# Kernel optimization log

Hardware: AMD Instinct MI355X
Metric: run time of the kernel (lower is better)

Reference implementation:

```python
import jax, jax.numpy as jnp
import numpy as np

N_NODES = 50000
N_EDGES = 800000
D = 128


def setup_inputs() -> dict:
    key = jax.random.key(0)
    ks = jax.random.split(key, 8)
    # xavier-uniform bound for [D, D]
    bound = np.sqrt(6.0 / (D + D)).astype(np.float32)
    x = jax.random.normal(ks[0], (N_NODES, D), dtype=jnp.float32)
    edge_index = jax.random.randint(ks[1], (2, N_EDGES), 0, N_NODES)
    W0 = jax.random.uniform(ks[2], (D, D), jnp.float32, -bound, bound)
    W1 = jax.random.uniform(ks[3], (D, D), jnp.float32, -bound, bound)
    W2 = jax.random.uniform(ks[4], (D, D), jnp.float32, -bound, bound)
    b0 = jnp.zeros((D,), jnp.float32)
    b1 = jnp.zeros((D,), jnp.float32)
    b2 = jnp.zeros((D,), jnp.float32)
    return {"x": x, "edge_index": edge_index,
            "W0": W0, "b0": b0, "W1": W1, "b1": b1, "W2": W2, "b2": b2}


def _gcn_conv(h, W, b, row, col, norm, n):
    # PyG GCNConv: x' = hat(D)^-1/2 hat(A) hat(D)^-1/2 (h W) + b
    hw = h @ W                                   # [N, D]
    msg = norm[:, None] * hw[row]                # gather from source nodes
    agg = jax.ops.segment_sum(msg, col, num_segments=n)  # scatter-add to targets
    return agg + b


def reference(x, edge_index, W0, b0, W1, b1, W2, b2):
    n = x.shape[0]
    loops = jnp.arange(n)
    # add self-loops (PyG GCNConv default)
    row = jnp.concatenate([edge_index[0], loops])
    col = jnp.concatenate([edge_index[1], loops])
    deg = jax.ops.segment_sum(jnp.ones(row.shape, x.dtype), col, num_segments=n)
    dinv = jnp.where(deg > 0, jax.lax.rsqrt(deg), 0.0)
    norm = dinv[row] * dinv[col]
    # dropout omitted (eval/inference mode)
    res = []
    h = x
    for W, b in ((W0, b0), (W1, b1), (W2, b2)):
        h = jnp.tanh(_gcn_conv(h, W, b, row, col, norm, n))
        res.append(h)
    return jnp.stack(res, axis=1)  # [N, n_layers, D]
```

## Files before the change

kernel.cpp:

```cpp
#include <hip/hip_runtime.h>
#include <math.h>

#define N_NODES 50000
#define N_EDGES 800000
#define D 128
#define NPAD 50048
#define NBLK 196

typedef unsigned int uint32;
typedef __attribute__((ext_vector_type(8))) short short8;
typedef __attribute__((ext_vector_type(4))) float f32x4;

__device__ __forceinline__ ushort f2bf(float f) {
    uint32 u = __float_as_uint(f);
    u = (u + 0x7fff + ((u >> 16) & 1)) >> 16;
    return (ushort)u;
}
__device__ __forceinline__ float bf2f(ushort u) {
    return __uint_as_float(((uint32)u) << 16);
}


__global__ __launch_bounds__(256) void k_count(const int* __restrict__ col,
                                               int* __restrict__ counts,
                                               int* __restrict__ rank_buf) {
    int i4 = (blockIdx.x * 256 + threadIdx.x) * 4;
    if (i4 < N_EDGES) {
        int4 c = *(const int4*)(col + i4);
        int4 r;
        r.x = atomicAdd(&counts[c.x], 1);
        r.y = atomicAdd(&counts[c.y], 1);
        r.z = atomicAdd(&counts[c.z], 1);
        r.w = atomicAdd(&counts[c.w], 1);
        *(int4*)(rank_buf + i4) = r;
    }
}

__global__ __launch_bounds__(256) void k_scan_local(const int* __restrict__ counts,
                                                    int* __restrict__ offsets,
                                                    int* __restrict__ partials) {
    __shared__ int wsum[4];
    int tid = threadIdx.x;
    int i = blockIdx.x * 256 + tid;
    int v = (i < N_NODES) ? counts[i] : 0;
    int lane = tid & 63, wv = tid >> 6;
    int x = v;
    #pragma unroll
    for (int off = 1; off < 64; off <<= 1) {
        int y = __shfl_up(x, off);
        if (lane >= off) x += y;
    }
    if (lane == 63) wsum[wv] = x;
    __syncthreads();
    int b0 = wsum[0], b1 = wsum[1], b2 = wsum[2], b3 = wsum[3];
    int base = (wv > 0 ? b0 : 0) + (wv > 1 ? b1 : 0) + (wv > 2 ? b2 : 0);
    if (i < N_NODES) offsets[i] = base + x - v;
    if (tid == 255) partials[blockIdx.x] = b0 + b1 + b2 + b3;
}

__global__ __launch_bounds__(256) void k_scan_add(int* __restrict__ offsets,
                                                  const int* __restrict__ partials,
                                                  const int* __restrict__ counts,
                                                  float* __restrict__ dinv) {
    __shared__ int wsum[4];
    int tid = threadIdx.x;
    int p = (tid < (int)blockIdx.x && tid < NBLK) ? partials[tid] : 0;
    int lane = tid & 63, wv = tid >> 6;
    #pragma unroll
    for (int off = 32; off; off >>= 1) p += __shfl_down(p, off);
    if (lane == 0) wsum[wv] = p;
    __syncthreads();
    int base = wsum[0] + wsum[1] + wsum[2] + wsum[3];
    int i = blockIdx.x * 256 + tid;
    if (i < N_NODES) {
        offsets[i] += base;
        dinv[i] = rsqrtf((float)counts[i] + 1.0f);
    }
    if (i == 0) offsets[N_NODES] = N_EDGES;
}

__global__ __launch_bounds__(256) void k_fill(const int* __restrict__ row,
                                              const int* __restrict__ col,
                                              const int* __restrict__ offsets,
                                              const int* __restrict__ rank_buf,
                                              int* __restrict__ csr_rows) {
    int i4 = (blockIdx.x * 256 + threadIdx.x) * 4;
    if (i4 < N_EDGES) {
        int4 c = *(const int4*)(col + i4);
        int4 r = *(const int4*)(rank_buf + i4);
        int4 rw = *(const int4*)(row + i4);
        csr_rows[offsets[c.x] + r.x] = rw.x;
        csr_rows[offsets[c.y] + r.y] = rw.y;
        csr_rows[offsets[c.z] + r.z] = rw.z;
        csr_rows[offsets[c.w] + r.w] = rw.w;
    }
}

#define BM 64
#define LDA 136
#define NTILES ((N_NODES + BM - 1) / BM)
#define GEMM_BLOCKS 512

__global__ __launch_bounds__(256) void k_gemm(const float* __restrict__ hf,
                                              const ushort* __restrict__ hb,
                                              const float* __restrict__ W,
                                              const float* __restrict__ dinv,
                                              ushort* __restrict__ hw) {
    __shared__ __align__(16) ushort As[BM * LDA];
    __shared__ __align__(16) ushort Wt[D * LDA];
    int tid = threadIdx.x;
    int lane = tid & 63;
    int w = tid >> 6;
    int quad = lane >> 4;
    int m16 = lane & 15;

    #pragma unroll 4
    for (int i = 0; i < 64; ++i) {
        int flat = tid + 256 * i;
        int k = flat >> 7, n = flat & 127;
        Wt[n * LDA + k] = f2bf(W[flat]);
    }

    for (int t = blockIdx.x; t < NTILES; t += GEMM_BLOCKS) {
        int row0 = t * BM;
        __syncthreads();

        {
            int base = tid * 32;
            int r = base >> 7, c = base & 127;
            int row = row0 + r;
            ushort* dst = As + r * LDA + c;
            if (hf) {
                if (row < N_NODES) {
                    const float4* src = (const float4*)(hf + (size_t)row * D + c);
                    #pragma unroll
                    for (int j = 0; j < 4; ++j) {
                        float4 v0 = src[2 * j], v1 = src[2 * j + 1];
                        ushort4 u0, u1;
                        u0.x = f2bf(v0.x); u0.y = f2bf(v0.y); u0.z = f2bf(v0.z); u0.w = f2bf(v0.w);
                        u1.x = f2bf(v1.x); u1.y = f2bf(v1.y); u1.z = f2bf(v1.z); u1.w = f2bf(v1.w);
                        *(ushort4*)(dst + 8 * j) = u0;
                        *(ushort4*)(dst + 8 * j + 4) = u1;
                    }
                } else {
                    short8 z = {};
                    #pragma unroll
                    for (int j = 0; j < 4; ++j) *(short8*)(dst + 8 * j) = z;
                }
            } else {
                if (row < N_NODES) {
                    const short8* src = (const short8*)(hb + (size_t)row * D + c);
                    #pragma unroll
                    for (int j = 0; j < 4; ++j) *(short8*)(dst + 8 * j) = src[j];
                } else {
                    short8 z = {};
                    #pragma unroll
                    for (int j = 0; j < 4; ++j) *(short8*)(dst + 8 * j) = z;
                }
            }
        }
        __syncthreads();

        f32x4 acc[8];
        #pragma unroll
        for (int ct = 0; ct < 8; ++ct) acc[ct] = (f32x4){0.f, 0.f, 0.f, 0.f};
        #pragma unroll
        for (int ks = 0; ks < 4; ++ks) {
            short8 a = *(const short8*)(As + (w * 16 + m16) * LDA + ks * 32 + quad * 8);
            #pragma unroll
            for (int ct = 0; ct < 8; ++ct) {
                short8 b = *(const short8*)(Wt + (ct * 16 + m16) * LDA + ks * 32 + quad * 8);
                acc[ct] = __builtin_amdgcn_mfma_f32_16x16x32_bf16(a, b, acc[ct], 0, 0, 0);
            }
        }

        float dv[4];
        #pragma unroll
        for (int r = 0; r < 4; ++r) {
            int row = row0 + w * 16 + quad * 4 + r;
            dv[r] = (row < N_NODES) ? dinv[row] : 0.f;
        }
        #pragma unroll
        for (int ct = 0; ct < 8; ++ct) {
            #pragma unroll
            for (int r = 0; r < 4; ++r)
                As[(w * 16 + quad * 4 + r) * LDA + ct * 16 + m16] = f2bf(acc[ct][r] * dv[r]);
        }
        #pragma unroll
        for (int i = 0; i < 4; ++i) {
            int chunk = i * 64 + lane;
            int r = chunk >> 4, c8 = chunk & 15;
            int row = row0 + w * 16 + r;
            if (row < N_NODES) {
                short8 v = *(const short8*)(As + (w * 16 + r) * LDA + c8 * 8);
                *(short8*)(hw + (size_t)row * D + c8 * 8) = v;
            }
        }
    }
}

__global__ __launch_bounds__(256) void k_agg(const ushort* __restrict__ hw,
                                             const float* __restrict__ dinv,
                                             const int* __restrict__ offsets,
                                             const int* __restrict__ csr_rows,
                                             const float* __restrict__ bias,
                                             float* __restrict__ out, int layer,
                                             ushort* __restrict__ hnext, int write_next) {
    int node = blockIdx.x * 4 + (threadIdx.x >> 6);
    int lane = threadIdx.x & 63;
    int h = lane >> 5;
    int ls = lane & 31;

    float4 acc = make_float4(0.f, 0.f, 0.f, 0.f);
    int s = offsets[node], e = offsets[node + 1];
    int j = s + h;
    for (; j + 6 < e; j += 8) {
        int r0 = csr_rows[j];
        int r1 = csr_rows[j + 2];
        int r2 = csr_rows[j + 4];
        int r3 = csr_rows[j + 6];
        ushort4 v0 = *((const ushort4*)(hw + (size_t)r0 * D) + ls);
        ushort4 v1 = *((const ushort4*)(hw + (size_t)r1 * D) + ls);
        ushort4 v2 = *((const ushort4*)(hw + (size_t)r2 * D) + ls);
        ushort4 v3 = *((const ushort4*)(hw + (size_t)r3 * D) + ls);
        acc.x += bf2f(v0.x) + bf2f(v1.x) + bf2f(v2.x) + bf2f(v3.x);
        acc.y += bf2f(v0.y) + bf2f(v1.y) + bf2f(v2.y) + bf2f(v3.y);
        acc.z += bf2f(v0.z) + bf2f(v1.z) + bf2f(v2.z) + bf2f(v3.z);
        acc.w += bf2f(v0.w) + bf2f(v1.w) + bf2f(v2.w) + bf2f(v3.w);
    }
    for (; j < e; j += 2) {
        int r = csr_rows[j];
        ushort4 v = *((const ushort4*)(hw + (size_t)r * D) + ls);
        acc.x += bf2f(v.x); acc.y += bf2f(v.y);
        acc.z += bf2f(v.z); acc.w += bf2f(v.w);
    }
    acc.x += __shfl_xor(acc.x, 32);
    acc.y += __shfl_xor(acc.y, 32);
    acc.z += __shfl_xor(acc.z, 32);
    acc.w += __shfl_xor(acc.w, 32);

    if (h == 0) {
        float di = dinv[node];
        ushort4 sv = *((const ushort4*)(hw + (size_t)node * D) + ls);
        float4 b = *((const float4*)bias + ls);
        float4 o;
        o.x = tanhf(di * (acc.x + bf2f(sv.x)) + b.x);
        o.y = tanhf(di * (acc.y + bf2f(sv.y)) + b.y);
        o.z = tanhf(di * (acc.z + bf2f(sv.z)) + b.z);
        o.w = tanhf(di * (acc.w + bf2f(sv.w)) + b.w);
        *((float4*)(out + ((size_t)node * 3 + layer) * D) + ls) = o;
        if (write_next) {
            ushort4 nv;
            nv.x = f2bf(o.x); nv.y = f2bf(o.y); nv.z = f2bf(o.z); nv.w = f2bf(o.w);
            *((ushort4*)(hnext + (size_t)node * D) + ls) = nv;
        }
    }
}


extern "C" void kernel_launch(void* const* d_in, const int* in_sizes, int n_in,
                              void* d_out, int out_size, void* d_ws, size_t ws_size,
                              hipStream_t stream) {
    const float* x  = (const float*)d_in[0];
    const int*   ei = (const int*)d_in[1];
    const float* W0 = (const float*)d_in[2];
    const float* b0 = (const float*)d_in[3];
    const float* W1 = (const float*)d_in[4];
    const float* b1 = (const float*)d_in[5];
    const float* W2 = (const float*)d_in[6];
    const float* b2 = (const float*)d_in[7];
    float* out = (float*)d_out;

    const int* row = ei;
    const int* col = ei + N_EDGES;

    float* dinv    = (float*)d_ws;
    int*   counts  = (int*)(dinv + NPAD);
    int*   offsets = counts + NPAD;
    int*   partials= offsets + NPAD;
    int*   rank_buf= partials + 256;
    int*   csr     = rank_buf + N_EDGES;
    ushort* hw     = (ushort*)(csr + N_EDGES);
    ushort* hnext  = hw + (size_t)NPAD * D;

    int nb_e4 = (N_EDGES / 4 + 255) / 256;

    hipMemsetAsync(counts, 0, NPAD * sizeof(int), stream);
    k_count<<<nb_e4, 256, 0, stream>>>(col, counts, rank_buf);
    k_scan_local<<<NBLK, 256, 0, stream>>>(counts, offsets, partials);
    k_scan_add<<<NBLK, 256, 0, stream>>>(offsets, partials, counts, dinv);
    k_fill<<<nb_e4, 256, 0, stream>>>(row, col, offsets, rank_buf, csr);

    int nb_agg = N_NODES / 4;

    const float* Ws_[3] = {W0, W1, W2};
    const float* bs_[3] = {b0, b1, b2};
    for (int l = 0; l < 3; ++l) {
        if (l == 0) k_gemm<<<GEMM_BLOCKS, 256, 0, stream>>>(x, (const ushort*)nullptr, Ws_[l], dinv, hw);
        else        k_gemm<<<GEMM_BLOCKS, 256, 0, stream>>>((const float*)nullptr, hnext, Ws_[l], dinv, hw);
        k_agg<<<nb_agg, 256, 0, stream>>>(hw, dinv, offsets, csr, bs_[l], out, l,
                                          hnext, l < 2 ? 1 : 0);
    }
}
```

Baseline: 309.0 us.

## Preconvert weights once, one-tile GEMM blocks with direct A loads, wider agg gathers

Adds a kernel that converts and transposes all three weight matrices to bf16 once, so each GEMM block copies ready-made bf16 rows into shared memory instead of converting fp32 per block. The GEMM now launches one block per 64-row tile and loads A fragments straight from global memory into registers, dropping the A staging through shared memory and one barrier. The aggregation kernel gathers 16-byte rows with four edge groups per wave instead of two, using a two-step shuffle reduction. Per-block weight setup is still repeated across many more blocks, and the agg change alters memory access granularity.

```diff
diff --git a/kernel.cpp b/kernel.cpp
--- a/kernel.cpp
+++ b/kernel.cpp
@@ -96,105 +96,94 @@
     }
 }
 
+__global__ __launch_bounds__(256) void k_wconv(const float* __restrict__ W0,
+                                               const float* __restrict__ W1,
+                                               const float* __restrict__ W2,
+                                               ushort* __restrict__ wt) {
+    int i = blockIdx.x * 256 + threadIdx.x;
+    int l = i >> 14;
+    int flat = i & 16383;
+    int n = flat >> 7, k = flat & 127;
+    const float* W = (l == 0) ? W0 : (l == 1) ? W1 : W2;
+    wt[i] = f2bf(W[k * 128 + n]);
+}
+
 #define BM 64
 #define LDA 136
 #define NTILES ((N_NODES + BM - 1) / BM)
-#define GEMM_BLOCKS 512
 
 __global__ __launch_bounds__(256) void k_gemm(const float* __restrict__ hf,
                                               const ushort* __restrict__ hb,
-                                              const float* __restrict__ W,
+                                              const ushort* __restrict__ wt,
                                               const float* __restrict__ dinv,
                                               ushort* __restrict__ hw) {
+    __shared__ __align__(16) ushort Wt[D * LDA];
     __shared__ __align__(16) ushort As[BM * LDA];
-    __shared__ __align__(16) ushort Wt[D * LDA];
     int tid = threadIdx.x;
     int lane = tid & 63;
     int w = tid >> 6;
     int quad = lane >> 4;
     int m16 = lane & 15;
 
-    #pragma unroll 4
-    for (int i = 0; i < 64; ++i) {
-        int flat = tid + 256 * i;
-        int k = flat >> 7, n = flat & 127;
-        Wt[n * LDA + k] = f2bf(W[flat]);
-    }
-
-    for (int t = blockIdx.x; t < NTILES; t += GEMM_BLOCKS) {
-        int row0 = t * BM;
-        __syncthreads();
-
-        {
-            int base = tid * 32;
-            int r = base >> 7, c = base & 127;
-            int row = row0 + r;
-            ushort* dst = As + r * LDA + c;
-            if (hf) {
-                if (row < N_NODES) {
-                    const float4* src = (const float4*)(hf + (size_t)row * D + c);
-                    #pragma unroll
-                    for (int j = 0; j < 4; ++j) {
-                        float4 v0 = src[2 * j], v1 = src[2 * j + 1];
-                        ushort4 u0, u1;
-                        u0.x = f2bf(v0.x); u0.y = f2bf(v0.y); u0.z = f2bf(v0.z); u0.w = f2bf(v0.w);
-                        u1.x = f2bf(v1.x); u1.y = f2bf(v1.y); u1.z = f2bf(v1.z); u1.w = f2bf(v1.w);
-                        *(ushort4*)(dst + 8 * j) = u0;
-                        *(ushort4*)(dst + 8 * j + 4) = u1;
-                    }
-                } else {
-                    short8 z = {};
-                    #pragma unroll
-                    for (int j = 0; j < 4; ++j) *(short8*)(dst + 8 * j) = z;
-                }
+    #pragma unroll
+    for (int i = 0; i < 8; ++i) {
+        int chunk = i * 256 + tid;
+        int n = chunk >> 4, k16 = chunk & 15;
+        *(short8*)(Wt + n * LDA + k16 * 8) = *(const short8*)(wt + n * 128 + k16 * 8);
+    }
+    __syncthreads();
+
+    int row0 = blockIdx.x * BM;
+    int arow = row0 + w * 16 + m16;
+
+    f32x4 acc[8];
+    #pragma unroll
+    for (int ct = 0; ct < 8; ++ct) acc[ct] = (f32x4){0.f, 0.f, 0.f, 0.f};
+
+    #pragma unroll
+    for (int ks = 0; ks < 4; ++ks) {
+        short8 a;
+        if (hf) {
+            if (arow < N_NODES) {
+                const float4* p = (const float4*)(hf + (size_t)arow * D + ks * 32 + quad * 8);
+                float4 x0 = p[0], x1 = p[1];
+                a[0] = (short)f2bf(x0.x); a[1] = (short)f2bf(x0.y);
+                a[2] = (short)f2bf(x0.z); a[3] = (short)f2bf(x0.w);
+                a[4] = (short)f2bf(x1.x); a[5] = (short)f2bf(x1.y);
+                a[6] = (short)f2bf(x1.z); a[7] = (short)f2bf(x1.w);
             } else {
-                if (row < N_NODES) {
-                    const short8* src = (const short8*)(hb + (size_t)row * D + c);
-                    #pragma unroll
-                    for (int j = 0; j < 4; ++j) *(short8*)(dst + 8 * j) = src[j];
-                } else {
-                    short8 z = {};
-                    #pragma unroll
-                    for (int j = 0; j < 4; ++j) *(short8*)(dst + 8 * j) = z;
-                }
+                a = (short8){};
             }
-        }
-        __syncthreads();
-
-        f32x4 acc[8];
-        #pragma unroll
-        for (int ct = 0; ct < 8; ++ct) acc[ct] = (f32x4){0.f, 0.f, 0.f, 0.f};
-        #pragma unroll
-        for (int ks = 0; ks < 4; ++ks) {
-            short8 a = *(const short8*)(As + (w * 16 + m16) * LDA + ks * 32 + quad * 8);
-            #pragma unroll
-            for (int ct = 0; ct < 8; ++ct) {
-                short8 b = *(const short8*)(Wt + (ct * 16 + m16) * LDA + ks * 32 + quad * 8);
-                acc[ct] = __builtin_amdgcn_mfma_f32_16x16x32_bf16(a, b, acc[ct], 0, 0, 0);
-            }
-        }
-
-        float dv[4];
-        #pragma unroll
-        for (int r = 0; r < 4; ++r) {
-            int row = row0 + w * 16 + quad * 4 + r;
-            dv[r] = (row < N_NODES) ? dinv[row] : 0.f;
+        } else {
+            a = *(const short8*)(hb + (size_t)arow * D + ks * 32 + quad * 8);
         }
         #pragma unroll
         for (int ct = 0; ct < 8; ++ct) {
-            #pragma unroll
-            for (int r = 0; r < 4; ++r)
-                As[(w * 16 + quad * 4 + r) * LDA + ct * 16 + m16] = f2bf(acc[ct][r] * dv[r]);
-        }
-        #pragma unroll
-        for (int i = 0; i < 4; ++i) {
-            int chunk = i * 64 + lane;
-            int r = chunk >> 4, c8 = chunk & 15;
-            int row = row0 + w * 16 + r;
-            if (row < N_NODES) {
-                short8 v = *(const short8*)(As + (w * 16 + r) * LDA + c8 * 8);
-                *(short8*)(hw + (size_t)row * D + c8 * 8) = v;
-            }
+            short8 b = *(const short8*)(Wt + (ct * 16 + m16) * LDA + ks * 32 + quad * 8);
+            acc[ct] = __builtin_amdgcn_mfma_f32_16x16x32_bf16(a, b, acc[ct], 0, 0, 0);
+        }
+    }
+
+    float dv[4];
+    #pragma unroll
+    for (int r = 0; r < 4; ++r) {
+        int row = row0 + w * 16 + quad * 4 + r;
+        dv[r] = (row < N_NODES) ? dinv[row] : 0.f;
+    }
+    #pragma unroll
+    for (int ct = 0; ct < 8; ++ct) {
+        #pragma unroll
+        for (int r = 0; r < 4; ++r)
+            As[(w * 16 + quad * 4 + r) * LDA + ct * 16 + m16] = f2bf(acc[ct][r] * dv[r]);
+    }
+    #pragma unroll
+    for (int i = 0; i < 4; ++i) {
+        int chunk = i * 64 + lane;
+        int r = chunk >> 4, c8 = chunk & 15;
+        int row = row0 + w * 16 + r;
+        if (row < N_NODES) {
+            short8 v = *(const short8*)(As + (w * 16 + r) * LDA + c8 * 8);
+            *(short8*)(hw + (size_t)row * D + c8 * 8) = v;
         }
     }
 }
@@ -208,51 +197,51 @@
                                              ushort* __restrict__ hnext, int write_next) {
     int node = blockIdx.x * 4 + (threadIdx.x >> 6);
     int lane = threadIdx.x & 63;
-    int h = lane >> 5;
-    int ls = lane & 31;
-
-    float4 acc = make_float4(0.f, 0.f, 0.f, 0.f);
+    int q = lane >> 4;
+    int m = lane & 15;
+
+    float acc[8] = {};
     int s = offsets[node], e = offsets[node + 1];
-    int j = s + h;
-    for (; j + 6 < e; j += 8) {
+    int j = s + q;
+    for (; j + 4 < e; j += 8) {
         int r0 = csr_rows[j];
-        int r1 = csr_rows[j + 2];
-        int r2 = csr_rows[j + 4];
-        int r3 = csr_rows[j + 6];
-        ushort4 v0 = *((const ushort4*)(hw + (size_t)r0 * D) + ls);
-        ushort4 v1 = *((const ushort4*)(hw + (size_t)r1 * D) + ls);
-        ushort4 v2 = *((const ushort4*)(hw + (size_t)r2 * D) + ls);
-        ushort4 v3 = *((const ushort4*)(hw + (size_t)r3 * D) + ls);
-        acc.x += bf2f(v0.x) + bf2f(v1.x) + bf2f(v2.x) + bf2f(v3.x);
-        acc.y += bf2f(v0.y) + bf2f(v1.y) + bf2f(v2.y) + bf2f(v3.y);
-        acc.z += bf2f(v0.z) + bf2f(v1.z) + bf2f(v2.z) + bf2f(v3.z);
-        acc.w += bf2f(v0.w) + bf2f(v1.w) + bf2f(v2.w) + bf2f(v3.w);
-    }
-    for (; j < e; j += 2) {
+        int r1 = csr_rows[j + 4];
+        short8 v0 = *((const short8*)(hw + (size_t)r0 * D) + m);
+        short8 v1 = *((const short8*)(hw + (size_t)r1 * D) + m);
+        #pragma unroll
+        for (int i = 0; i < 8; ++i)
+            acc[i] += bf2f((ushort)v0[i]) + bf2f((ushort)v1[i]);
+    }
+    for (; j < e; j += 4) {
         int r = csr_rows[j];
-        ushort4 v = *((const ushort4*)(hw + (size_t)r * D) + ls);
-        acc.x += bf2f(v.x); acc.y += bf2f(v.y);
-        acc.z += bf2f(v.z); acc.w += bf2f(v.w);
-    }
-    acc.x += __shfl_xor(acc.x, 32);
-    acc.y += __shfl_xor(acc.y, 32);
-    acc.z += __shfl_xor(acc.z, 32);
-    acc.w += __shfl_xor(acc.w, 32);
-
-    if (h == 0) {
+        short8 v = *((const short8*)(hw + (size_t)r * D) + m);
+        #pragma unroll
+        for (int i = 0; i < 8; ++i) acc[i] += bf2f((ushort)v[i]);
+    }
+    #pragma unroll
+    for (int i = 0; i < 8; ++i) {
+        acc[i] += __shfl_xor(acc[i], 16);
+        acc[i] += __shfl_xor(acc[i], 32);
+    }
+
+    if (q == 0) {
         float di = dinv[node];
-        ushort4 sv = *((const ushort4*)(hw + (size_t)node * D) + ls);
-        float4 b = *((const float4*)bias + ls);
-        float4 o;
-        o.x = tanhf(di * (acc.x + bf2f(sv.x)) + b.x);
-        o.y = tanhf(di * (acc.y + bf2f(sv.y)) + b.y);
-        o.z = tanhf(di * (acc.z + bf2f(sv.z)) + b.z);
-        o.w = tanhf(di * (acc.w + bf2f(sv.w)) + b.w);
-        *((float4*)(out + ((size_t)node * 3 + layer) * D) + ls) = o;
+        short8 sv = *((const short8*)(hw + (size_t)node * D) + m);
+        float4 ba = ((const float4*)bias)[2 * m];
+        float4 bb = ((const float4*)bias)[2 * m + 1];
+        float bv[8] = {ba.x, ba.y, ba.z, ba.w, bb.x, bb.y, bb.z, bb.w};
+        float o[8];
+        #pragma unroll
+        for (int i = 0; i < 8; ++i)
+            o[i] = tanhf(di * (acc[i] + bf2f((ushort)sv[i])) + bv[i]);
+        float* op = out + ((size_t)node * 3 + layer) * D;
+        ((float4*)op)[2 * m]     = make_float4(o[0], o[1], o[2], o[3]);
+        ((float4*)op)[2 * m + 1] = make_float4(o[4], o[5], o[6], o[7]);
         if (write_next) {
-            ushort4 nv;
-            nv.x = f2bf(o.x); nv.y = f2bf(o.y); nv.z = f2bf(o.z); nv.w = f2bf(o.w);
-            *((ushort4*)(hnext + (size_t)node * D) + ls) = nv;
+            short8 nv;
+            #pragma unroll
+            for (int i = 0; i < 8; ++i) nv[i] = (short)f2bf(o[i]);
+            *((short8*)(hnext + (size_t)node * D) + m) = nv;
         }
     }
 }
@@ -274,18 +263,20 @@
     const int* row = ei;
     const int* col = ei + N_EDGES;
 
-    float* dinv    = (float*)d_ws;
-    int*   counts  = (int*)(dinv + NPAD);
-    int*   offsets = counts + NPAD;
-    int*   partials= offsets + NPAD;
-    int*   rank_buf= partials + 256;
-    int*   csr     = rank_buf + N_EDGES;
-    ushort* hw     = (ushort*)(csr + N_EDGES);
-    ushort* hnext  = hw + (size_t)NPAD * D;
+    float*  dinv    = (float*)d_ws;
+    int*    counts  = (int*)(dinv + NPAD);
+    int*    offsets = counts + NPAD;
+    int*    partials= offsets + NPAD;
+    ushort* wt      = (ushort*)(partials + 256);
+    int*    rank_buf= (int*)(wt + 3 * 16384);
+    int*    csr     = rank_buf + N_EDGES;
+    ushort* hw      = (ushort*)(csr + N_EDGES);
+    ushort* hnext   = hw + (size_t)NPAD * D;
 
     int nb_e4 = (N_EDGES / 4 + 255) / 256;
 
     hipMemsetAsync(counts, 0, NPAD * sizeof(int), stream);
+    k_wconv<<<192, 256, 0, stream>>>(W0, W1, W2, wt);
     k_count<<<nb_e4, 256, 0, stream>>>(col, counts, rank_buf);
     k_scan_local<<<NBLK, 256, 0, stream>>>(counts, offsets, partials);
     k_scan_add<<<NBLK, 256, 0, stream>>>(offsets, partials, counts, dinv);
@@ -293,11 +284,10 @@
 
     int nb_agg = N_NODES / 4;
 
-    const float* Ws_[3] = {W0, W1, W2};
     const float* bs_[3] = {b0, b1, b2};
     for (int l = 0; l < 3; ++l) {
-        if (l == 0) k_gemm<<<GEMM_BLOCKS, 256, 0, stream>>>(x, (const ushort*)nullptr, Ws_[l], dinv, hw);
-        else        k_gemm<<<GEMM_BLOCKS, 256, 0, stream>>>((const float*)nullptr, hnext, Ws_[l], dinv, hw);
+        if (l == 0) k_gemm<<<NTILES, 256, 0, stream>>>(x, (const ushort*)nullptr, wt, dinv, hw);
+        else        k_gemm<<<NTILES, 256, 0, stream>>>((const float*)nullptr, hnext, wt + l * 16384, dinv, hw);
         k_agg<<<nb_agg, 256, 0, stream>>>(hw, dinv, offsets, csr, bs_[l], out, l,
                                           hnext, l < 2 ? 1 : 0);
     }
```

Result: no change. 312.7 us (+1.2%).
